# Optimization experiments

Hardware: AMD Instinct MI355X
Metric: run time of the kernel (lower is better)

Reference implementation:

```python
import math
import jax, jax.numpy as jnp
import numpy as np

H = 8
D = 32  # c_hidden per head


def setup_inputs() -> dict:
    key = jax.random.key(0)
    ks = jax.random.split(key, 10)
    B, Q, K, C = 2, 2048, 2048, 256
    s = 1.0 / math.sqrt(C)
    return {
        "q_x": jax.random.normal(ks[0], (B, Q, C), jnp.float32),
        "kv_x": jax.random.normal(ks[1], (B, K, C), jnp.float32),
        "bias_mask": jax.random.normal(ks[2], (B, 1, 1, K), jnp.float32),
        "bias_pair": jax.random.normal(ks[3], (1, H, Q, K), jnp.float32),
        "Wq": jax.random.normal(ks[4], (H * D, C), jnp.float32) * s,
        "Wk": jax.random.normal(ks[5], (H * D, C), jnp.float32) * s,
        "Wv": jax.random.normal(ks[6], (H * D, C), jnp.float32) * s,
        "Wo": jax.random.normal(ks[7], (C, H * D), jnp.float32) * s,
        "bo": jnp.zeros((C,), jnp.float32),
        "Wg": jax.random.normal(ks[8], (H * D, C), jnp.float32) * s,
        "bg": jnp.zeros((H * D,), jnp.float32),
    }


def reference(q_x, kv_x, bias_mask, bias_pair, Wq, Wk, Wv, Wo, bo, Wg, bg):
    B, Q, C = q_x.shape
    K = kv_x.shape[-2]
    # projections (torch Linear: x @ W.T), split heads -> [B,H,L,D]
    q = (q_x @ Wq.T).reshape(B, Q, H, D).swapaxes(-2, -3) / math.sqrt(D)
    k = (kv_x @ Wk.T).reshape(B, K, H, D).swapaxes(-2, -3)
    v = (kv_x @ Wv.T).reshape(B, K, H, D).swapaxes(-2, -3)
    scores = jnp.einsum("bhqd,bhkd->bhqk", q, k) + bias_mask + bias_pair
    w = jax.nn.softmax(scores, axis=-1)
    o = jnp.einsum("bhqk,bhkd->bhqd", w, v).swapaxes(-2, -3)  # [B,Q,H,D]
    g = jax.nn.sigmoid(q_x @ Wg.T + bg).reshape(B, Q, H, D)
    o = o * g
    return o.reshape(B, Q, H * D) @ Wo.T + bo
```

## Files before the change

### kernel.cpp

```cpp
#include <hip/hip_runtime.h>
#include <hip/hip_bf16.h>
#include <stdint.h>
#include <math.h>

typedef __attribute__((ext_vector_type(8))) short bf16x8;
typedef __attribute__((ext_vector_type(4))) float f32x4;

#define HQ 2048
#define HK 2048
#define NH 8
#define ND 32
#define NC 256

union U8 { uint32_t u[4]; bf16x8 v; };

__device__ __forceinline__ uint16_t f2bf(float f) {
  uint32_t u = __float_as_uint(f);
  u += 0x7FFFu + ((u >> 16) & 1u);
  return (uint16_t)(u >> 16);
}
__device__ __forceinline__ uint32_t pack2bf(float a, float b) {
  return (uint32_t)f2bf(a) | ((uint32_t)f2bf(b) << 16);
}
__device__ __forceinline__ int swz64(int row, int piece) {
  int s = (((row >> 3) & 1) << 1) | ((row >> 1) & 1);
  return row * 64 + ((piece ^ s) << 4);
}
__device__ __forceinline__ f32x4 mfma32(bf16x8 a, bf16x8 b, f32x4 c) {
  return __builtin_amdgcn_mfma_f32_16x16x32_bf16(a, b, c, 0, 0, 0);
}
__device__ __forceinline__ void dma16(const void* g, void* l) {
  __builtin_amdgcn_global_load_lds(
      (const __attribute__((address_space(1))) uint32_t*)g,
      (__attribute__((address_space(3))) uint32_t*)l, 16, 0, 0);
}

__global__ __launch_bounds__(256) void proj_kernel(
    const float* __restrict__ qx, const float* __restrict__ kvx,
    const float* __restrict__ Wq, const float* __restrict__ Wk,
    const float* __restrict__ Wv, const float* __restrict__ Wg,
    const float* __restrict__ bg,
    uint16_t* __restrict__ q_p, uint16_t* __restrict__ k_p,
    uint16_t* __restrict__ v_p, float* __restrict__ g_ws)
{
  const int bx = blockIdx.x;
  const int Mb = bx & 63, Nb = (bx >> 6) & 3, p = bx >> 8;
  const int Mbase = Mb * 64, Nbase = Nb * 64;
  const float* X = (p == 0 || p == 3) ? qx : kvx;
  const float* W = (p == 0) ? Wq : (p == 1) ? Wk : (p == 2) ? Wv : Wg;

  __shared__ __align__(16) uint16_t smem[4096];
  uint16_t* sX = smem;
  uint16_t* sW = smem + 2048;

  const int tid = threadIdx.x;
  const int l = tid & 63, w = tid >> 6;
  const int qq = l & 15, g = l >> 4;
  const int row = tid >> 2, gp = tid & 3;

  f32x4 acc[4] = {};

  for (int ks = 0; ks < 8; ++ks) {
    const float* xs = X + (size_t)(Mbase + row) * 256 + ks * 32 + gp * 8;
    f32x4 x0 = *(const f32x4*)xs;
    f32x4 x1 = *(const f32x4*)(xs + 4);
    const float* ws_ = W + (size_t)(Nbase + row) * 256 + ks * 32 + gp * 8;
    f32x4 w0 = *(const f32x4*)ws_;
    f32x4 w1 = *(const f32x4*)(ws_ + 4);
    U8 ux, uw;
    ux.u[0] = pack2bf(x0[0], x0[1]); ux.u[1] = pack2bf(x0[2], x0[3]);
    ux.u[2] = pack2bf(x1[0], x1[1]); ux.u[3] = pack2bf(x1[2], x1[3]);
    uw.u[0] = pack2bf(w0[0], w0[1]); uw.u[1] = pack2bf(w0[2], w0[3]);
    uw.u[2] = pack2bf(w1[0], w1[1]); uw.u[3] = pack2bf(w1[2], w1[3]);
    __syncthreads();
    *(bf16x8*)((char*)sX + swz64(row, gp)) = ux.v;
    *(bf16x8*)((char*)sW + swz64(row, gp)) = uw.v;
    __syncthreads();
    bf16x8 a = *(bf16x8*)((char*)sX + swz64(w * 16 + qq, g));
#pragma unroll
    for (int nf = 0; nf < 4; ++nf) {
      bf16x8 bb = *(bf16x8*)((char*)sW + swz64(nf * 16 + qq, g));
      acc[nf] = mfma32(a, bb, acc[nf]);
    }
  }

  if (p == 2) {
    __syncthreads();
#pragma unroll
    for (int nf = 0; nf < 4; ++nf) {
      int n_loc = nf * 16 + qq;
#pragma unroll
      for (int r = 0; r < 4; ++r) {
        int m_loc = w * 16 + 4 * g + r;
        int byte = n_loc * 128 + ((((m_loc >> 3) ^ (n_loc & 7)) << 4)) + (m_loc & 7) * 2;
        *(uint16_t*)((char*)smem + byte) = f2bf(acc[nf][r]);
      }
    }
    __syncthreads();
    const int n_loc = tid >> 2, mp = tid & 3;
    const int ng = Nbase + n_loc;
    const int hh = ng >> 5, dd = ng & 31;
    const int bb_ = Mbase >> 11;
#pragma unroll
    for (int jj = 0; jj < 2; ++jj) {
      int piece = mp * 2 + jj;
      bf16x8 vv = *(bf16x8*)((char*)smem + n_loc * 128 + ((piece ^ (n_loc & 7)) << 4));
      int seq = (Mbase & 2047) + piece * 8;
      *(bf16x8*)(v_p + ((size_t)(bb_ * NH + hh) * ND + dd) * (size_t)HK + seq) = vv;
    }
    return;
  }

#pragma unroll
  for (int nf = 0; nf < 4; ++nf) {
    int n = Nbase + nf * 16 + qq;
#pragma unroll
    for (int r = 0; r < 4; ++r) {
      int m = Mbase + w * 16 + 4 * g + r;
      float val = acc[nf][r];
      if (p == 0) {
        val *= 0.17677669529663687f;
        int bb_ = m >> 11, seq = m & 2047, hh = n >> 5, dd = n & 31;
        q_p[((size_t)(bb_ * NH + hh) * HQ + seq) * ND + dd] = f2bf(val);
      } else if (p == 1) {
        int bb_ = m >> 11, seq = m & 2047, hh = n >> 5, dd = n & 31;
        k_p[((size_t)(bb_ * NH + hh) * HK + seq) * ND + dd] = f2bf(val);
      } else {
        g_ws[(size_t)m * NC + n] = 1.f / (1.f + __expf(-(val + bg[n])));
      }
    }
  }
}

__global__ __launch_bounds__(256, 4) void attn_kernel(
    const uint16_t* __restrict__ q_p, const uint16_t* __restrict__ k_p,
    const uint16_t* __restrict__ v_p, const float* __restrict__ bias_mask,
    const float* __restrict__ bias_pair,
    float* __restrict__ O_ws, float* __restrict__ l_ws)
{
  const int bx = blockIdx.x;
  const int kh = bx & 1, h = (bx >> 1) & 7, qt = bx >> 4;

  __shared__ __align__(16) char LDS[40960];
  char* sK = LDS;
  char* sV = LDS + 8192;
  char* sP = LDS + 16384;
  char* sBM = LDS + 32768;

  const int tid = threadIdx.x;
  const int l = tid & 63, wq = tid >> 6;
  const int qq = l & 15, g = l >> 4;
  const int bsel = wq >> 1, hsel = wq & 1;
  const int q_glob = qt * 64 + wq * 16 + qq;

  bf16x8 qf0 = *(const bf16x8*)(q_p + ((size_t)h * HQ + q_glob) * ND + g * 8);
  bf16x8 qf1 = *(const bf16x8*)(q_p + ((size_t)(NH + h) * HQ + q_glob) * ND + g * 8);

  const char* kSrc;
  {
    int B = hsel * 1024 + l * 16;
    int Lr = B >> 7, cpos = l & 7;
    int hp = cpos ^ (Lr & 7);
    int half = hp >> 2, pc = hp & 3;
    int s = Lr * 2 + half, F = s >> 4, qs = s & 15;
    int krow = 8 * (qs >> 2) + (qs & 3) + 4 * F;
    kSrc = (const char*)k_p + (size_t)(bsel * NH + h) * HK * ND * 2
           + kh * 65536 + krow * 64 + pc * 16;
  }
  const char* vSrc;
  {
    int B = hsel * 1024 + l * 16;
    int d = B >> 6, cpos = l & 3;
    int gs = cpos ^ ((d ^ (d >> 2)) & 3);
    vSrc = (const char*)v_p + (size_t)(bsel * NH + h) * ND * (size_t)HK * 2
           + kh * 2048 + (size_t)d * (HK * 2) + gs * 16;
  }
  const char* pSrc0; const char* pSrc1;
  {
    const char* bpBlk = (const char*)bias_pair
        + ((size_t)h * HQ + qt * 64) * (size_t)HK * 4 + kh * 4096;
#define BP_SRC(jj) ({ int row = wq * 16 + (jj) * 8 + (l >> 3); \
                      int gs = (l & 7) ^ (row & 7); \
                      bpBlk + (size_t)row * (HK * 4) + gs * 16; })
    pSrc0 = BP_SRC(0); pSrc1 = BP_SRC(1);
#undef BP_SRC
  }

  int afOff[2], vaOff[2], bpOff[2];
#pragma unroll
  for (int F = 0; F < 2; ++F) {
    int Lr = 8 * F + (qq >> 1);
    afOff[F] = Lr * 128 + ((((qq & 1) * 4 + g) ^ (Lr & 7)) << 4);
  }
#pragma unroll
  for (int hd = 0; hd < 2; ++hd) {
    int d = hd * 16 + qq;
    vaOff[hd] = d * 64 + (((g ^ ((d ^ (d >> 2)) & 3))) << 4);
  }
#pragma unroll
  for (int F = 0; F < 2; ++F) {
    int row = wq * 16 + qq;
    bpOff[F] = row * 128 + (((2 * g + F) ^ (row & 7)) << 4);
  }

#define STAGE(tt, dbi) do { \
    dma16(kSrc + (size_t)(tt) * 2048, sK + (dbi) * 4096 + bsel * 2048 + hsel * 1024); \
    dma16(vSrc + (size_t)(tt) * 64,   sV + (dbi) * 4096 + bsel * 2048 + hsel * 1024); \
    dma16(pSrc0 + (size_t)(tt) * 128, sP + (dbi) * 8192 + wq * 2048); \
    dma16(pSrc1 + (size_t)(tt) * 128, sP + (dbi) * 8192 + wq * 2048 + 1024); \
  } while (0)

  f32x4 o00 = {}, o01 = {}, o10 = {}, o11 = {};
  float l0 = 0.f, l1 = 0.f;

  dma16((const char*)bias_mask + kh * 4096 + wq * 1024 + l * 16,
        sBM + wq * 1024);
  dma16((const char*)bias_mask + 8192 + kh * 4096 + wq * 1024 + l * 16,
        sBM + 4096 + wq * 1024);
  STAGE(0, 0);

#pragma unroll 1
  for (int t = 0; t < 32; ++t) {
    const int bi = t & 1;
    if (t < 31) {
      STAGE(t + 1, bi ^ 1);
      asm volatile("s_waitcnt vmcnt(4)" ::: "memory");
    } else {
      asm volatile("s_waitcnt vmcnt(0)" ::: "memory");
    }
    __builtin_amdgcn_s_barrier();
    __builtin_amdgcn_sched_barrier(0);

    const char* bP = sP + bi * 8192;
    f32x4 bp0 = *(const f32x4*)(bP + bpOff[0]);
    f32x4 bp1 = *(const f32x4*)(bP + bpOff[1]);
    const int bmOff = t * 128 + 32 * g;

    {
      const char* bK = sK + bi * 4096;
      const char* bV = sV + bi * 4096;
      bf16x8 af0 = *(const bf16x8*)(bK + afOff[0]);
      bf16x8 af1 = *(const bf16x8*)(bK + afOff[1]);
      f32x4 z = {};
      f32x4 s0 = mfma32(af0, qf0, z);
      f32x4 s1 = mfma32(af1, qf0, z);
      f32x4 bm0 = *(const f32x4*)(sBM + bmOff);
      f32x4 bm1 = *(const f32x4*)(sBM + bmOff + 16);
#pragma unroll
      for (int r = 0; r < 4; ++r) {
        s0[r] += bp0[r] + bm0[r];
        s1[r] += bp1[r] + bm1[r];
      }
      U8 bu;
      {
        float p0 = __expf(s0[0]), p1 = __expf(s0[1]);
        float p2 = __expf(s0[2]), p3 = __expf(s0[3]);
        l0 += (p0 + p1) + (p2 + p3);
        bu.u[0] = pack2bf(p0, p1); bu.u[1] = pack2bf(p2, p3);
        p0 = __expf(s1[0]); p1 = __expf(s1[1]);
        p2 = __expf(s1[2]); p3 = __expf(s1[3]);
        l0 += (p0 + p1) + (p2 + p3);
        bu.u[2] = pack2bf(p0, p1); bu.u[3] = pack2bf(p2, p3);
      }
      bf16x8 va0 = *(const bf16x8*)(bV + vaOff[0]);
      bf16x8 va1 = *(const bf16x8*)(bV + vaOff[1]);
      o00 = mfma32(va0, bu.v, o00);
      o01 = mfma32(va1, bu.v, o01);
    }
    {
      const char* bK = sK + bi * 4096 + 2048;
      const char* bV = sV + bi * 4096 + 2048;
      bf16x8 af0 = *(const bf16x8*)(bK + afOff[0]);
      bf16x8 af1 = *(const bf16x8*)(bK + afOff[1]);
      f32x4 z = {};
      f32x4 s0 = mfma32(af0, qf1, z);
      f32x4 s1 = mfma32(af1, qf1, z);
      f32x4 bm0 = *(const f32x4*)(sBM + 4096 + bmOff);
      f32x4 bm1 = *(const f32x4*)(sBM + 4096 + bmOff + 16);
#pragma unroll
      for (int r = 0; r < 4; ++r) {
        s0[r] += bp0[r] + bm0[r];
        s1[r] += bp1[r] + bm1[r];
      }
      U8 bu;
      {
        float p0 = __expf(s0[0]), p1 = __expf(s0[1]);
        float p2 = __expf(s0[2]), p3 = __expf(s0[3]);
        l1 += (p0 + p1) + (p2 + p3);
        bu.u[0] = pack2bf(p0, p1); bu.u[1] = pack2bf(p2, p3);
        p0 = __expf(s1[0]); p1 = __expf(s1[1]);
        p2 = __expf(s1[2]); p3 = __expf(s1[3]);
        l1 += (p0 + p1) + (p2 + p3);
        bu.u[2] = pack2bf(p0, p1); bu.u[3] = pack2bf(p2, p3);
      }
      bf16x8 va0 = *(const bf16x8*)(bV + vaOff[0]);
      bf16x8 va1 = *(const bf16x8*)(bV + vaOff[1]);
      o10 = mfma32(va0, bu.v, o10);
      o11 = mfma32(va1, bu.v, o11);
    }

    __builtin_amdgcn_sched_barrier(0);
    __builtin_amdgcn_s_barrier();
  }
#undef STAGE

  l0 += __shfl_xor(l0, 16, 64);
  l0 += __shfl_xor(l0, 32, 64);
  l1 += __shfl_xor(l1, 16, 64);
  l1 += __shfl_xor(l1, 32, 64);
#pragma unroll
  for (int b = 0; b < 2; ++b) {
    f32x4 oa = b ? o10 : o00;
    f32x4 ob = b ? o11 : o01;
    float lr = b ? l1 : l0;
    __syncthreads();
    float* se = (float*)LDS + wq * 576;
#pragma unroll
    for (int r = 0; r < 4; ++r) {
      se[qq * 36 + 4 * g + r]      = oa[r];
      se[qq * 36 + 16 + 4 * g + r] = ob[r];
    }
    if (g == 0) l_ws[kh * 32768 + b * 16384 + h * 2048 + q_glob] = lr;
    __syncthreads();
    const int qrow = l >> 2, pc = l & 3;
    const float* sr = (float*)LDS + wq * 576 + qrow * 36 + pc * 8;
    f32x4 x0 = *(const f32x4*)sr;
    f32x4 x1 = *(const f32x4*)(sr + 4);
    const int q_out = qt * 64 + wq * 16 + qrow;
    float* dst = O_ws + ((size_t)((kh * 2 + b) * HQ + q_out)) * NC + h * ND + pc * 8;
    *(f32x4*)dst = x0;
    *(f32x4*)(dst + 4) = x1;
  }
}

__global__ __launch_bounds__(256) void outproj_kernel(
    const float* __restrict__ O_ws, const float* __restrict__ l_ws,
    const float* __restrict__ g_ws, const float* __restrict__ Wo,
    const float* __restrict__ bo, float* __restrict__ out)
{
  const int bx = blockIdx.x;
  const int Mb = bx & 63, Nb = bx >> 6;
  const int Mbase = Mb * 64, Nbase = Nb * 64;
  __shared__ __align__(16) uint16_t smem2[4096];
  uint16_t* sA = smem2;
  uint16_t* sB = smem2 + 2048;
  const int tid = threadIdx.x;
  const int l = tid & 63, w = tid >> 6;
  const int qq = l & 15, g = l >> 4;
  const int row = tid >> 2, gp = tid & 3;
  const int m = Mbase + row, bb2 = m >> 11, qloc = m & 2047;
  f32x4 acc[4] = {};
  for (int ks = 0; ks < 8; ++ks) {
    const size_t lidx = (size_t)bb2 * 16384 + (size_t)ks * 2048 + qloc;
    const float inv = 1.f / (l_ws[lidx] + l_ws[32768 + lidx]);
    const int col = ks * 32 + gp * 8;
    const float* o0p = O_ws + ((size_t)(bb2 * HQ + qloc)) * NC + col;
    const float* o1p = O_ws + ((size_t)((2 + bb2) * HQ + qloc)) * NC + col;
    const float* gpp = g_ws + ((size_t)(bb2 * HQ + qloc)) * NC + col;
    f32x4 a0 = *(const f32x4*)o0p;      f32x4 a1 = *(const f32x4*)(o0p + 4);
    f32x4 b0 = *(const f32x4*)o1p;      f32x4 b1 = *(const f32x4*)(o1p + 4);
    f32x4 g0 = *(const f32x4*)gpp;      f32x4 g1 = *(const f32x4*)(gpp + 4);
#pragma unroll
    for (int r = 0; r < 4; ++r) {
      a0[r] = (a0[r] + b0[r]) * inv * g0[r];
      a1[r] = (a1[r] + b1[r]) * inv * g1[r];
    }
    const float* wsrc = Wo + (size_t)(Nbase + row) * 256 + ks * 32 + gp * 8;
    f32x4 w0 = *(const f32x4*)wsrc;
    f32x4 w1 = *(const f32x4*)(wsrc + 4);
    U8 ua, uw;
    ua.u[0] = pack2bf(a0[0], a0[1]); ua.u[1] = pack2bf(a0[2], a0[3]);
    ua.u[2] = pack2bf(a1[0], a1[1]); ua.u[3] = pack2bf(a1[2], a1[3]);
    uw.u[0] = pack2bf(w0[0], w0[1]); uw.u[1] = pack2bf(w0[2], w0[3]);
    uw.u[2] = pack2bf(w1[0], w1[1]); uw.u[3] = pack2bf(w1[2], w1[3]);
    __syncthreads();
    *(bf16x8*)((char*)sA + swz64(row, gp)) = ua.v;
    *(bf16x8*)((char*)sB + swz64(row, gp)) = uw.v;
    __syncthreads();
    bf16x8 a = *(bf16x8*)((char*)sA + swz64(w * 16 + qq, g));
#pragma unroll
    for (int nf = 0; nf < 4; ++nf) {
      bf16x8 bb = *(bf16x8*)((char*)sB + swz64(nf * 16 + qq, g));
      acc[nf] = mfma32(a, bb, acc[nf]);
    }
  }
#pragma unroll
  for (int nf = 0; nf < 4; ++nf) {
    int n = Nbase + nf * 16 + qq;
    float bias = bo[n];
#pragma unroll
    for (int r = 0; r < 4; ++r) {
      int mm = Mbase + w * 16 + 4 * g + r;
      out[(size_t)mm * NC + n] = acc[nf][r] + bias;
    }
  }
}

extern "C" void kernel_launch(void* const* d_in, const int* in_sizes, int n_in,
                              void* d_out, int out_size, void* d_ws, size_t ws_size,
                              hipStream_t stream) {
  (void)in_sizes; (void)n_in; (void)out_size; (void)ws_size;
  const float* qx        = (const float*)d_in[0];
  const float* kvx       = (const float*)d_in[1];
  const float* bias_mask = (const float*)d_in[2];
  const float* bias_pair = (const float*)d_in[3];
  const float* Wq        = (const float*)d_in[4];
  const float* Wk        = (const float*)d_in[5];
  const float* Wv        = (const float*)d_in[6];
  const float* Wo        = (const float*)d_in[7];
  const float* bo        = (const float*)d_in[8];
  const float* Wg        = (const float*)d_in[9];
  const float* bg        = (const float*)d_in[10];

  char* ws = (char*)d_ws;
  uint16_t* q_p  = (uint16_t*)(ws);
  uint16_t* k_p  = (uint16_t*)(ws + (2u << 20));
  uint16_t* v_p  = (uint16_t*)(ws + (4u << 20));
  float*    g_ws = (float*)   (ws + (6u << 20));
  float*    O_ws = (float*)   (ws + (10u << 20));
  float*    l_ws = (float*)   (ws + (18u << 20));
  float* out = (float*)d_out;

  proj_kernel<<<dim3(1024), dim3(256), 0, stream>>>(qx, kvx, Wq, Wk, Wv, Wg, bg,
                                                    q_p, k_p, v_p, g_ws);
  attn_kernel<<<dim3(512), dim3(256), 0, stream>>>(q_p, k_p, v_p, bias_mask,
                                                   bias_pair, O_ws, l_ws);
  outproj_kernel<<<dim3(256), dim3(256), 0, stream>>>(O_ws, l_ws, g_ws, Wo, bo, out);
}
```

Baseline: 58.39 us.

## Split attention keys four ways with 512-thread blocks covering 128 queries

The attention kernel now uses 8 waves per block covering 128 query rows, and splits the key range into four chunks instead of two. Each block runs 16 iterations instead of 32. K and V staging is divided between wave groups, so each K/V tile loaded into LDS is shared by twice as many queries. The output projection kernel now sums four partial O and l buffers, which adds workspace traffic, LDS use and per-block register pressure in exchange for more reuse and a shorter sequential loop.

```diff
diff --git a/kernel.cpp b/kernel.cpp
--- a/kernel.cpp
+++ b/kernel.cpp
@@ -132,53 +132,58 @@
   }
 }
 
-__global__ __launch_bounds__(256, 4) void attn_kernel(
+__global__ __launch_bounds__(512, 4) void attn_kernel(
     const uint16_t* __restrict__ q_p, const uint16_t* __restrict__ k_p,
     const uint16_t* __restrict__ v_p, const float* __restrict__ bias_mask,
     const float* __restrict__ bias_pair,
     float* __restrict__ O_ws, float* __restrict__ l_ws)
 {
   const int bx = blockIdx.x;
-  const int kh = bx & 1, h = (bx >> 1) & 7, qt = bx >> 4;
-
-  __shared__ __align__(16) char LDS[40960];
+  const int khq = bx & 3, h = (bx >> 2) & 7, qt = bx >> 5;
+
+  __shared__ __align__(16) char LDS[57344];
   char* sK = LDS;
   char* sV = LDS + 8192;
   char* sP = LDS + 16384;
-  char* sBM = LDS + 32768;
+  char* sBM = LDS + 49152;
 
   const int tid = threadIdx.x;
   const int l = tid & 63, wq = tid >> 6;
   const int qq = l & 15, g = l >> 4;
-  const int bsel = wq >> 1, hsel = wq & 1;
-  const int q_glob = qt * 64 + wq * 16 + qq;
+  const int q_glob = qt * 128 + wq * 16 + qq;
 
   bf16x8 qf0 = *(const bf16x8*)(q_p + ((size_t)h * HQ + q_glob) * ND + g * 8);
   bf16x8 qf1 = *(const bf16x8*)(q_p + ((size_t)(NH + h) * HQ + q_glob) * ND + g * 8);
 
-  const char* kSrc;
-  {
+  const int rw = wq & 3;
+  const int bsel = rw >> 1, hsel = rw & 1;
+  const char* roleSrc;
+  int roleStride;
+  char* roleDst;
+  if (wq < 4) {
     int B = hsel * 1024 + l * 16;
     int Lr = B >> 7, cpos = l & 7;
     int hp = cpos ^ (Lr & 7);
     int half = hp >> 2, pc = hp & 3;
     int s = Lr * 2 + half, F = s >> 4, qs = s & 15;
     int krow = 8 * (qs >> 2) + (qs & 3) + 4 * F;
-    kSrc = (const char*)k_p + (size_t)(bsel * NH + h) * HK * ND * 2
-           + kh * 65536 + krow * 64 + pc * 16;
-  }
-  const char* vSrc;
-  {
+    roleSrc = (const char*)k_p + (size_t)(bsel * NH + h) * HK * ND * 2
+              + khq * 32768 + krow * 64 + pc * 16;
+    roleStride = 2048;
+    roleDst = sK + bsel * 2048 + hsel * 1024;
+  } else {
     int B = hsel * 1024 + l * 16;
     int d = B >> 6, cpos = l & 3;
     int gs = cpos ^ ((d ^ (d >> 2)) & 3);
-    vSrc = (const char*)v_p + (size_t)(bsel * NH + h) * ND * (size_t)HK * 2
-           + kh * 2048 + (size_t)d * (HK * 2) + gs * 16;
+    roleSrc = (const char*)v_p + (size_t)(bsel * NH + h) * ND * (size_t)HK * 2
+              + khq * 1024 + (size_t)d * (HK * 2) + gs * 16;
+    roleStride = 64;
+    roleDst = sV + bsel * 2048 + hsel * 1024;
   }
   const char* pSrc0; const char* pSrc1;
   {
     const char* bpBlk = (const char*)bias_pair
-        + ((size_t)h * HQ + qt * 64) * (size_t)HK * 4 + kh * 4096;
+        + ((size_t)h * HQ + qt * 128) * (size_t)HK * 4 + khq * 2048;
 #define BP_SRC(jj) ({ int row = wq * 16 + (jj) * 8 + (l >> 3); \
                       int gs = (l & 7) ^ (row & 7); \
                       bpBlk + (size_t)row * (HK * 4) + gs * 16; })
@@ -202,36 +207,37 @@
     int row = wq * 16 + qq;
     bpOff[F] = row * 128 + (((2 * g + F) ^ (row & 7)) << 4);
   }
+  const char* sBMr = sBM + (wq >> 2) * 4096;
 
 #define STAGE(tt, dbi) do { \
-    dma16(kSrc + (size_t)(tt) * 2048, sK + (dbi) * 4096 + bsel * 2048 + hsel * 1024); \
-    dma16(vSrc + (size_t)(tt) * 64,   sV + (dbi) * 4096 + bsel * 2048 + hsel * 1024); \
-    dma16(pSrc0 + (size_t)(tt) * 128, sP + (dbi) * 8192 + wq * 2048); \
-    dma16(pSrc1 + (size_t)(tt) * 128, sP + (dbi) * 8192 + wq * 2048 + 1024); \
+    dma16(roleSrc + (size_t)(tt) * roleStride, roleDst + (dbi) * 4096); \
+    dma16(pSrc0 + (size_t)(tt) * 128, sP + (dbi) * 16384 + wq * 2048); \
+    dma16(pSrc1 + (size_t)(tt) * 128, sP + (dbi) * 16384 + wq * 2048 + 1024); \
   } while (0)
 
   f32x4 o00 = {}, o01 = {}, o10 = {}, o11 = {};
   float l0 = 0.f, l1 = 0.f;
 
-  dma16((const char*)bias_mask + kh * 4096 + wq * 1024 + l * 16,
-        sBM + wq * 1024);
-  dma16((const char*)bias_mask + 8192 + kh * 4096 + wq * 1024 + l * 16,
-        sBM + 4096 + wq * 1024);
+  {
+    int p = wq & 3;
+    dma16((const char*)bias_mask + (p >> 1) * 8192 + khq * 2048 + (p & 1) * 1024 + l * 16,
+          sBM + (wq >> 2) * 4096 + p * 1024);
+  }
   STAGE(0, 0);
 
 #pragma unroll 1
-  for (int t = 0; t < 32; ++t) {
+  for (int t = 0; t < 16; ++t) {
     const int bi = t & 1;
-    if (t < 31) {
+    if (t < 15) {
       STAGE(t + 1, bi ^ 1);
-      asm volatile("s_waitcnt vmcnt(4)" ::: "memory");
+      asm volatile("s_waitcnt vmcnt(3)" ::: "memory");
     } else {
       asm volatile("s_waitcnt vmcnt(0)" ::: "memory");
     }
     __builtin_amdgcn_s_barrier();
     __builtin_amdgcn_sched_barrier(0);
 
-    const char* bP = sP + bi * 8192;
+    const char* bP = sP + bi * 16384;
     f32x4 bp0 = *(const f32x4*)(bP + bpOff[0]);
     f32x4 bp1 = *(const f32x4*)(bP + bpOff[1]);
     const int bmOff = t * 128 + 32 * g;
@@ -244,8 +250,8 @@
       f32x4 z = {};
       f32x4 s0 = mfma32(af0, qf0, z);
       f32x4 s1 = mfma32(af1, qf0, z);
-      f32x4 bm0 = *(const f32x4*)(sBM + bmOff);
-      f32x4 bm1 = *(const f32x4*)(sBM + bmOff + 16);
+      f32x4 bm0 = *(const f32x4*)(sBMr + bmOff);
+      f32x4 bm1 = *(const f32x4*)(sBMr + bmOff + 16);
 #pragma unroll
       for (int r = 0; r < 4; ++r) {
         s0[r] += bp0[r] + bm0[r];
@@ -275,8 +281,8 @@
       f32x4 z = {};
       f32x4 s0 = mfma32(af0, qf1, z);
       f32x4 s1 = mfma32(af1, qf1, z);
-      f32x4 bm0 = *(const f32x4*)(sBM + 4096 + bmOff);
-      f32x4 bm1 = *(const f32x4*)(sBM + 4096 + bmOff + 16);
+      f32x4 bm0 = *(const f32x4*)(sBMr + 2048 + bmOff);
+      f32x4 bm1 = *(const f32x4*)(sBMr + 2048 + bmOff + 16);
 #pragma unroll
       for (int r = 0; r < 4; ++r) {
         s0[r] += bp0[r] + bm0[r];
@@ -320,14 +326,14 @@
       se[qq * 36 + 4 * g + r]      = oa[r];
       se[qq * 36 + 16 + 4 * g + r] = ob[r];
     }
-    if (g == 0) l_ws[kh * 32768 + b * 16384 + h * 2048 + q_glob] = lr;
+    if (g == 0) l_ws[khq * 32768 + b * 16384 + h * 2048 + q_glob] = lr;
     __syncthreads();
     const int qrow = l >> 2, pc = l & 3;
     const float* sr = (float*)LDS + wq * 576 + qrow * 36 + pc * 8;
     f32x4 x0 = *(const f32x4*)sr;
     f32x4 x1 = *(const f32x4*)(sr + 4);
-    const int q_out = qt * 64 + wq * 16 + qrow;
-    float* dst = O_ws + ((size_t)((kh * 2 + b) * HQ + q_out)) * NC + h * ND + pc * 8;
+    const int q_out = qt * 128 + wq * 16 + qrow;
+    float* dst = O_ws + ((size_t)((khq * 2 + b) * HQ + q_out)) * NC + h * ND + pc * 8;
     *(f32x4*)dst = x0;
     *(f32x4*)(dst + 4) = x1;
   }
@@ -351,19 +357,25 @@
   const int m = Mbase + row, bb2 = m >> 11, qloc = m & 2047;
   f32x4 acc[4] = {};
   for (int ks = 0; ks < 8; ++ks) {
-    const size_t lidx = (size_t)bb2 * 16384 + (size_t)ks * 2048 + qloc;
-    const float inv = 1.f / (l_ws[lidx] + l_ws[32768 + lidx]);
+    const size_t lbase = (size_t)bb2 * 16384 + (size_t)ks * 2048 + qloc;
+    const float inv = 1.f / (l_ws[lbase] + l_ws[32768 + lbase] +
+                             l_ws[65536 + lbase] + l_ws[98304 + lbase]);
     const int col = ks * 32 + gp * 8;
-    const float* o0p = O_ws + ((size_t)(bb2 * HQ + qloc)) * NC + col;
-    const float* o1p = O_ws + ((size_t)((2 + bb2) * HQ + qloc)) * NC + col;
+    f32x4 a0 = {}, a1 = {};
+#pragma unroll
+    for (int kq = 0; kq < 4; ++kq) {
+      const float* op = O_ws + ((size_t)((kq * 2 + bb2) * HQ + qloc)) * NC + col;
+      f32x4 t0 = *(const f32x4*)op;
+      f32x4 t1 = *(const f32x4*)(op + 4);
+#pragma unroll
+      for (int r = 0; r < 4; ++r) { a0[r] += t0[r]; a1[r] += t1[r]; }
+    }
     const float* gpp = g_ws + ((size_t)(bb2 * HQ + qloc)) * NC + col;
-    f32x4 a0 = *(const f32x4*)o0p;      f32x4 a1 = *(const f32x4*)(o0p + 4);
-    f32x4 b0 = *(const f32x4*)o1p;      f32x4 b1 = *(const f32x4*)(o1p + 4);
     f32x4 g0 = *(const f32x4*)gpp;      f32x4 g1 = *(const f32x4*)(gpp + 4);
 #pragma unroll
     for (int r = 0; r < 4; ++r) {
-      a0[r] = (a0[r] + b0[r]) * inv * g0[r];
-      a1[r] = (a1[r] + b1[r]) * inv * g1[r];
+      a0[r] = a0[r] * inv * g0[r];
+      a1[r] = a1[r] * inv * g1[r];
     }
     const float* wsrc = Wo + (size_t)(Nbase + row) * 256 + ks * 32 + gp * 8;
     f32x4 w0 = *(const f32x4*)wsrc;
@@ -418,12 +430,12 @@
   uint16_t* v_p  = (uint16_t*)(ws + (4u << 20));
   float*    g_ws = (float*)   (ws + (6u << 20));
   float*    O_ws = (float*)   (ws + (10u << 20));
-  float*    l_ws = (float*)   (ws + (18u << 20));
+  float*    l_ws = (float*)   (ws + (26u << 20));
   float* out = (float*)d_out;
 
   proj_kernel<<<dim3(1024), dim3(256), 0, stream>>>(qx, kvx, Wq, Wk, Wv, Wg, bg,
                                                     q_p, k_p, v_p, g_ws);
-  attn_kernel<<<dim3(512), dim3(256), 0, stream>>>(q_p, k_p, v_p, bias_mask,
+  attn_kernel<<<dim3(512), dim3(512), 0, stream>>>(q_p, k_p, v_p, bias_mask,
                                                    bias_pair, O_ws, l_ws);
   outproj_kernel<<<dim3(256), dim3(256), 0, stream>>>(O_ws, l_ws, g_ws, Wo, bo, out);
 }
```

Measured after the change: 55.57 us. 1.05x faster.
